# Kernel optimization log

Hardware: AMD Instinct MI355X
Metric: run time of the kernel (lower is better)

## Reference

```python
import jax, jax.numpy as jnp
import numpy as np

N, E, H, K, C, NMOD = 50000, 600000, 128, 5, 60, 12  # nodes, edges, hidden, hops, classes, 6 blocks * 2 modules


def setup_inputs() -> dict:
    key = jax.random.key(0)
    ks = iter(jax.random.split(key, 48))
    def rn(shape, scale=0.05):
        return jax.random.normal(next(ks), shape, jnp.float32) * scale
    return {
        "node_features": rn((N, 2), 1.0),
        "lap_pe": rn((N, K), 1.0),
        "edge_feat": rn((E, 4), 1.0),
        "src": jax.random.randint(next(ks), (E,), 0, N),
        "dst": jax.random.randint(next(ks), (E,), 0, N),
        "in_w": rn((2, H)), "in_b": jnp.zeros((H,), jnp.float32),
        "pos_w": rn((K, H)), "pos_b": jnp.zeros((H,), jnp.float32),
        "edge_w": rn((4, H)), "edge_b": jnp.zeros((H,), jnp.float32),
        "conv_w": rn((NMOD, 2, (K + 1) * H, H)), "conv_b": jnp.zeros((NMOD, 2, H), jnp.float32),
        "bn_g": jnp.ones((NMOD, 2, H), jnp.float32), "bn_b": jnp.zeros((NMOD, 2, H), jnp.float32),
        "ff_w": rn((NMOD, H, H)), "ff_b": jnp.zeros((NMOD, H), jnp.float32),
        "pose_w1": rn((H, H)), "pose_b1": jnp.zeros((H,), jnp.float32),
        "pose_w2": rn((H, 3)), "pose_b2": jnp.zeros((3,), jnp.float32),
        "lab_w1": rn((H, H)), "lab_b1": jnp.zeros((H,), jnp.float32),
        "lab_w2": rn((H, C)), "lab_b2": jnp.zeros((C,), jnp.float32),
    }


def _bn(x, g, b):
    # BatchNorm1d in training mode: stats over node axis
    m = x.mean(0)
    v = x.var(0)
    return (x - m) * jax.lax.rsqrt(v + 1e-5) * g + b


def reference(node_features, lap_pe, edge_feat, src, dst,
              in_w, in_b, pos_w, pos_b, edge_w, edge_b,
              conv_w, conv_b, bn_g, bn_b, ff_w, ff_b,
              pose_w1, pose_b1, pose_w2, pose_b2,
              lab_w1, lab_b1, lab_w2, lab_b2):
    seg = jax.ops.segment_sum
    # symmetric degree norm (in-degree, clamped to 1) as in DGL TAGConv
    deg = seg(jnp.ones((E,), node_features.dtype), dst, num_segments=N)
    norm = jnp.clip(deg, 1.0) ** -0.5  # [N]

    # edge feature aggregation: copy_e -> sum onto dst
    agg_e = seg(edge_feat @ edge_w + edge_b, dst, num_segments=N)  # [N,H]
    h = node_features @ in_w + in_b + lap_pe @ pos_w + pos_b + agg_e

    def tagconv(x, W, b):
        # fstack = [x, Ax, ..., A^K x] with A = D^-1/2 A D^-1/2, then single linear
        fs = [x]
        for _ in range(K):
            z = fs[-1] * norm[:, None]
            z = seg(z[src], dst, num_segments=N) * norm[:, None]
            fs.append(z)
        return jnp.concatenate(fs, axis=-1) @ W + b  # [N,H]

    for m in range(NMOD):  # 6 blocks x 2 TAGConvModules, sequential
        h_in = h
        h = jax.nn.relu(_bn(tagconv(h, conv_w[m, 0], conv_b[m, 0]), bn_g[m, 0], bn_b[m, 0]))
        h = jax.nn.relu(_bn(tagconv(h, conv_w[m, 1], conv_b[m, 1]), bn_g[m, 1], bn_b[m, 1]))
        h = h @ ff_w[m] + ff_b[m] + h_in  # dropout = identity (eval)

    pose = jax.nn.relu(h @ pose_w1 + pose_b1) @ pose_w2 + pose_b2  # [N,3]
    y = h.mean(0)  # dgl.mean_nodes (single batched graph)
    labels = jax.nn.relu(y @ lab_w1 + lab_b1) @ lab_w2 + lab_b2  # [C]
    return pose, labels
```

## Files before the change

### kernel.cpp

```cpp
#include <hip/hip_runtime.h>

#define NN 50000
#define EE 600000
#define HH 128
#define KK 5
#define CC 60
#define NMODS 12
#define MAXPE 750080
#define SC_NB 49

typedef _Float16 f16;
typedef __attribute__((ext_vector_type(8))) _Float16 f16x8;
typedef __attribute__((ext_vector_type(4))) _Float16 f16x4;
typedef __attribute__((ext_vector_type(16))) float f32x16;
typedef __attribute__((ext_vector_type(4))) int int4v;
typedef __attribute__((ext_vector_type(4))) float f32x4;

#define ZSL ((size_t)NN * 128)

#define GLOBAL_AS __attribute__((address_space(1)))
#define LDS_AS __attribute__((address_space(3)))


__global__ void k_deg(const int* __restrict__ dst, int* __restrict__ deg) {
    int i = blockIdx.x * 256 + threadIdx.x;
    if (i < EE) atomicAdd(&deg[dst[i]], 1);
}

__global__ __launch_bounds__(256) void k_scan1(const int* __restrict__ deg,
                                               int* __restrict__ rs, int* __restrict__ bsum) {
    __shared__ int sm[256];
    int t = threadIdx.x;
    int base = blockIdx.x * 1024 + t * 4;
    int d[4];
#pragma unroll
    for (int j = 0; j < 4; j++) {
        int i = base + j;
        d[j] = (i < NN) ? ((deg[i] + 3) & ~3) : 0;
    }
    int sum = d[0] + d[1] + d[2] + d[3];
    sm[t] = sum;
    __syncthreads();
    for (int off = 1; off < 256; off <<= 1) {
        int v = (t >= off) ? sm[t - off] : 0;
        __syncthreads();
        sm[t] += v;
        __syncthreads();
    }
    int excl = sm[t] - sum;
    int run = excl;
#pragma unroll
    for (int j = 0; j < 4; j++) {
        int i = base + j;
        if (i < NN) rs[i] = run;
        run += d[j];
    }
    if (t == 255) bsum[blockIdx.x] = sm[t];
}

__global__ __launch_bounds__(64) void k_scan2(const int* __restrict__ bsum, int* __restrict__ binc) {
    int l = threadIdx.x;
    int v = (l < SC_NB) ? bsum[l] : 0;
#pragma unroll
    for (int off = 1; off < 64; off <<= 1) {
        int tv = __shfl_up(v, off, 64);
        if (l >= off) v += tv;
    }
    binc[l] = v;
}

__global__ __launch_bounds__(256) void k_scan3(const int* __restrict__ binc, int* __restrict__ rs) {
    int i = blockIdx.x * 256 + threadIdx.x;
    if (i < NN) {
        int b = i >> 10;
        if (b > 0) rs[i] += binc[b - 1];
    } else if (i == NN) {
        rs[NN] = binc[SC_NB - 1];
    }
}

__global__ void k_norm(const int* __restrict__ deg, float* __restrict__ norm) {
    int i = blockIdx.x * 256 + threadIdx.x;
    if (i < NN) {
        int d = deg[i];
        float fd = (float)(d < 1 ? 1 : d);
        norm[i] = 1.0f / sqrtf(fd);
    }
}

__global__ void k_fill(const int* __restrict__ src, const int* __restrict__ dst,
                       const int* __restrict__ rs, const float* __restrict__ norm,
                       int* __restrict__ cursor,
                       int* __restrict__ csrc, float* __restrict__ ew, int* __restrict__ ceid) {
    int i = blockIdx.x * 256 + threadIdx.x;
    if (i >= EE) return;
    int d = dst[i];
    int slot = atomicAdd(&cursor[d], 1);
    int p = rs[d] + slot;
    int s = src[i];
    csrc[p] = s;
    ew[p] = norm[s];
    ceid[p] = i;
}


__global__ void k_cvtw(const float* __restrict__ conv_w, const float* __restrict__ ff_w,
                       const float* __restrict__ pose_w1,
                       f16* __restrict__ wc, f16* __restrict__ wf, f16* __restrict__ wp) {
    int i = blockIdx.x * 256 + threadIdx.x;
    const int NCW = 24 * 128 * 768;
    const int NFW = 12 * 128 * 128;
    const int NPW = 128 * 128;
    if (i < NCW) {
        int mat = i / (128 * 768); int rem = i - mat * (128 * 768);
        int col = rem / 768; int k = rem - col * 768;
        wc[i] = (f16)conv_w[(size_t)mat * 768 * 128 + (size_t)k * 128 + col];
    } else if (i < NCW + NFW) {
        int j = i - NCW;
        int mat = j / (128 * 128); int rem = j - mat * (128 * 128);
        int col = rem / 128; int k = rem - col * 128;
        wf[j] = (f16)ff_w[(size_t)mat * 128 * 128 + k * 128 + col];
    } else if (i < NCW + NFW + NPW) {
        int j = i - NCW - NFW;
        int col = j / 128; int k = j - col * 128;
        wp[j] = (f16)pose_w1[k * 128 + col];
    }
}


__global__ __launch_bounds__(128) void k_h0(
    const float* __restrict__ nf, const float* __restrict__ pe, const float* __restrict__ ef,
    const int* __restrict__ rs, const int* __restrict__ ceid, const float* __restrict__ ew,
    const int* __restrict__ deg,
    const float* __restrict__ in_w, const float* __restrict__ in_b,
    const float* __restrict__ pos_w, const float* __restrict__ pos_b,
    const float* __restrict__ edge_w, const float* __restrict__ edge_b,
    float* __restrict__ h, f16* __restrict__ zc) {
    int n = blockIdx.x;
    int f = threadIdx.x;
    float v = in_b[f] + pos_b[f];
    v += nf[n * 2 + 0] * in_w[f] + nf[n * 2 + 1] * in_w[HH + f];
#pragma unroll
    for (int k = 0; k < KK; k++) v += pe[n * KK + k] * pos_w[k * HH + f];
    float e0 = edge_w[f], e1 = edge_w[HH + f], e2 = edge_w[2 * HH + f], e3 = edge_w[3 * HH + f];
    int s = rs[n], e = rs[n + 1];
    v += (float)deg[n] * edge_b[f];
    for (int i = s; i < e; i++) {
        if (ew[i] == 0.f) continue;
        int eid = ceid[i];
        float4 x = ((const float4*)ef)[eid];
        v += x.x * e0 + x.y * e1 + x.z * e2 + x.w * e3;
    }
    h[(size_t)n * HH + f] = v;
    zc[(size_t)n * 128 + f] = (f16)v;
}


__global__ __launch_bounds__(256) void k_prop16(
    const f16* __restrict__ zin, f16* __restrict__ zout,
    const float* __restrict__ norm, const int* __restrict__ rs,
    const int* __restrict__ csrc, const float* __restrict__ ew) {
    int tid = threadIdx.x;
    int n = blockIdx.x * 16 + (tid >> 4);
    if (n >= NN) return;
    int c = (tid & 15) * 8;
    int s = rs[n], e = rs[n + 1];
    const f16* zp = zin + c;
    float acc[8] = {0.f, 0.f, 0.f, 0.f, 0.f, 0.f, 0.f, 0.f};
    for (int i = s; i < e; i += 4) {
        int4v id4 = __builtin_nontemporal_load((const int4v*)(csrc + i));
        f32x4 w4 = __builtin_nontemporal_load((const f32x4*)(ew + i));
        f16x8 v0 = *(const f16x8*)(zp + (size_t)id4.x * 128);
        f16x8 v1 = *(const f16x8*)(zp + (size_t)id4.y * 128);
        f16x8 v2 = *(const f16x8*)(zp + (size_t)id4.z * 128);
        f16x8 v3 = *(const f16x8*)(zp + (size_t)id4.w * 128);
#pragma unroll
        for (int j = 0; j < 8; j++)
            acc[j] += (float)v0[j] * w4.x + (float)v1[j] * w4.y +
                      (float)v2[j] * w4.z + (float)v3[j] * w4.w;
    }
    float nw = norm[n];
    f16x8 o;
#pragma unroll
    for (int j = 0; j < 8; j++) o[j] = (f16)(acc[j] * nw);
    *(f16x8*)(zout + (size_t)n * 128 + c) = o;
}


template <int KT, int BIAS, int RESID, int RELU, int WRZ>
__global__ __launch_bounds__(256) void k_mm(
    const f16* __restrict__ A, const f16* __restrict__ Wt,
    const float* __restrict__ bias, const float* __restrict__ Rsd,
    float* __restrict__ Y, f16* __restrict__ Zout) {
    __shared__ char smem[65536];
    char* As = smem;
    char* Bs = smem + 32768;
    int tid = threadIdx.x;
    int lane = tid & 63;
    int w = tid >> 6, wm = w >> 1, wn = w & 1;
    int n0 = blockIdx.x * 128;
    f32x16 acc[2][2] = {};
    for (int k0 = 0; k0 < KT; k0 += 128) {
        __syncthreads();
        const f16* Asl = A + (size_t)(k0 >> 7) * ZSL;
#pragma unroll
        for (int i = 0; i < 8; i++) {
            int p = (i * 256 + tid) * 16;
            int o = p ^ (((p >> 8) & 15) << 4);
            int r = o >> 8, ce = (o & 255) >> 1;
            int row = n0 + r; if (row >= NN) row = 0;
            const f16* ga = Asl + (size_t)row * 128 + ce;
            char* lba = As + i * 4096 + w * 1024;
            __builtin_amdgcn_global_load_lds((const GLOBAL_AS void*)ga, (LDS_AS void*)lba, 16, 0, 0);
            const f16* gb = Wt + (size_t)r * KT + k0 + ce;
            char* lbb = Bs + i * 4096 + w * 1024;
            __builtin_amdgcn_global_load_lds((const GLOBAL_AS void*)gb, (LDS_AS void*)lbb, 16, 0, 0);
        }
        asm volatile("s_waitcnt vmcnt(0)" ::: "memory");
        __syncthreads();
#pragma unroll
        for (int s = 0; s < 8; s++) {
            int koff = s * 32 + (lane >> 5) * 16;
            f16x8 a[2], b[2];
#pragma unroll
            for (int m = 0; m < 2; m++) {
                int rl = wm * 64 + m * 32 + (lane & 31);
                int oa = (rl * 256 + koff) ^ ((rl & 15) << 4);
                a[m] = *(const f16x8*)(As + oa);
                int cl = wn * 64 + m * 32 + (lane & 31);
                int ob = (cl * 256 + koff) ^ ((cl & 15) << 4);
                b[m] = *(const f16x8*)(Bs + ob);
            }
#pragma unroll
            for (int m = 0; m < 2; m++)
#pragma unroll
                for (int nb = 0; nb < 2; nb++)
                    acc[m][nb] = __builtin_amdgcn_mfma_f32_32x32x16_f16(a[m], b[nb], acc[m][nb], 0, 0, 0);
        }
    }
#pragma unroll
    for (int m = 0; m < 2; m++) {
        int rb = n0 + wm * 64 + m * 32 + 4 * (lane >> 5);
#pragma unroll
        for (int nb = 0; nb < 2; nb++) {
            int col = wn * 64 + nb * 32 + (lane & 31);
            float bv = 0.f;
            if (BIAS) bv = bias[col];
#pragma unroll
            for (int r = 0; r < 16; r++) {
                int row = rb + (r & 3) + 8 * (r >> 2);
                if (row >= NN) continue;
                float v = acc[m][nb][r] + bv;
                if (RESID) v += Rsd[(size_t)row * HH + col];
                if (RELU) v = fmaxf(v, 0.f);
                Y[(size_t)row * HH + col] = v;
                if (WRZ) Zout[(size_t)row * 128 + col] = (f16)v;
            }
        }
    }
}


__global__ __launch_bounds__(256) void k_bnstats(const float* __restrict__ Y, float* __restrict__ part) {
    int tid = threadIdx.x;
    float s = 0.f, q = 0.f;
    for (int n = blockIdx.x * 2 + (tid >> 7); n < NN; n += 512) {
        float v = Y[(size_t)n * HH + (tid & 127)];
        s += v; q += v * v;
    }
    __shared__ float sh[512];
    sh[tid] = s; sh[256 + tid] = q;
    __syncthreads();
    if (tid < 128) {
        part[blockIdx.x * 256 + tid] = sh[tid] + sh[tid + 128];
        part[blockIdx.x * 256 + 128 + tid] = sh[256 + tid] + sh[256 + tid + 128];
    }
}

__global__ __launch_bounds__(128) void k_bnfin(const float* __restrict__ part,
                                               const float* __restrict__ g, const float* __restrict__ b,
                                               float* __restrict__ sc, float* __restrict__ sh) {
    int f = threadIdx.x;
    float s = 0.f, q = 0.f;
    for (int bi = 0; bi < 256; bi++) {
        s += part[bi * 256 + f];
        q += part[bi * 256 + 128 + f];
    }
    float mean = s / (float)NN;
    float var = q / (float)NN - mean * mean;
    float scale = g[f] / sqrtf(var + 1e-5f);
    sc[f] = scale;
    sh[f] = b[f] - mean * scale;
}

__global__ __launch_bounds__(256) void k_bnapply(const float* __restrict__ Y,
                                                 const float* __restrict__ sc, const float* __restrict__ sh,
                                                 f16* __restrict__ zc) {
    int idx = blockIdx.x * 256 + threadIdx.x;
    if (idx >= NN * 32) return;
    float4 v = ((const float4*)Y)[idx];
    int c = idx & 31;
    float4 a = ((const float4*)sc)[c];
    float4 b = ((const float4*)sh)[c];
    int n = idx >> 5;
    f16x4 o;
    o[0] = (f16)fmaxf(v.x * a.x + b.x, 0.f);
    o[1] = (f16)fmaxf(v.y * a.y + b.y, 0.f);
    o[2] = (f16)fmaxf(v.z * a.z + b.z, 0.f);
    o[3] = (f16)fmaxf(v.w * a.w + b.w, 0.f);
    *(f16x4*)(zc + (size_t)n * 128 + c * 4) = o;
}


__global__ __launch_bounds__(128) void k_pose2(const float* __restrict__ T,
                                               const float* __restrict__ W2, const float* __restrict__ b2,
                                               float* __restrict__ out) {
    int tid = threadIdx.x;
    int n = blockIdx.x * 4 + (tid >> 5);
    int c = tid & 31;
    float4 tv = ((const float4*)T)[(size_t)n * 32 + c];
    float p0 = 0.f, p1 = 0.f, p2 = 0.f;
#pragma unroll
    for (int i = 0; i < 4; i++) {
        float t = (i == 0) ? tv.x : (i == 1) ? tv.y : (i == 2) ? tv.z : tv.w;
        int k = c * 4 + i;
        p0 += t * W2[k * 3 + 0];
        p1 += t * W2[k * 3 + 1];
        p2 += t * W2[k * 3 + 2];
    }
#pragma unroll
    for (int off = 16; off > 0; off >>= 1) {
        p0 += __shfl_down(p0, off, 32);
        p1 += __shfl_down(p1, off, 32);
        p2 += __shfl_down(p2, off, 32);
    }
    if (c == 0) {
        out[(size_t)n * 3 + 0] = p0 + b2[0];
        out[(size_t)n * 3 + 1] = p1 + b2[1];
        out[(size_t)n * 3 + 2] = p2 + b2[2];
    }
}

__global__ __launch_bounds__(256) void k_meanpart(const float* __restrict__ Y, float* __restrict__ part) {
    int tid = threadIdx.x;
    float s = 0.f;
    for (int n = blockIdx.x * 2 + (tid >> 7); n < NN; n += 512) {
        s += Y[(size_t)n * HH + (tid & 127)];
    }
    __shared__ float sh[256];
    sh[tid] = s;
    __syncthreads();
    if (tid < 128) part[blockIdx.x * 128 + tid] = sh[tid] + sh[tid + 128];
}

__global__ __launch_bounds__(128) void k_labels(const float* __restrict__ part,
                                                const float* __restrict__ w1, const float* __restrict__ b1,
                                                const float* __restrict__ w2, const float* __restrict__ b2,
                                                float* __restrict__ out) {
    __shared__ float ym[128];
    __shared__ float t2[128];
    int f = threadIdx.x;
    float s = 0.f;
    for (int bi = 0; bi < 256; bi++) s += part[bi * 128 + f];
    ym[f] = s / (float)NN;
    __syncthreads();
    float a = b1[f];
    for (int k = 0; k < 128; k++) a += ym[k] * w1[k * 128 + f];
    t2[f] = fmaxf(a, 0.f);
    __syncthreads();
    if (f < CC) {
        float a2 = b2[f];
        for (int k = 0; k < 128; k++) a2 += t2[k] * w2[k * CC + f];
        out[(size_t)NN * 3 + f] = a2;
    }
}


static inline size_t align256(size_t x) { return (x + 255) & ~(size_t)255; }

extern "C" void kernel_launch(void* const* d_in, const int* in_sizes, int n_in,
                              void* d_out, int out_size, void* d_ws, size_t ws_size,
                              hipStream_t stream) {
    const float* nf = (const float*)d_in[0];
    const float* pe = (const float*)d_in[1];
    const float* ef = (const float*)d_in[2];
    const int* src = (const int*)d_in[3];
    const int* dst = (const int*)d_in[4];
    const float* in_w = (const float*)d_in[5];
    const float* in_b = (const float*)d_in[6];
    const float* pos_w = (const float*)d_in[7];
    const float* pos_b = (const float*)d_in[8];
    const float* edge_w = (const float*)d_in[9];
    const float* edge_b = (const float*)d_in[10];
    const float* conv_w = (const float*)d_in[11];
    const float* bn_g = (const float*)d_in[13];
    const float* bn_b = (const float*)d_in[14];
    const float* ff_w = (const float*)d_in[15];
    const float* ff_b = (const float*)d_in[16];
    const float* pose_w1 = (const float*)d_in[17];
    const float* pose_b1 = (const float*)d_in[18];
    const float* pose_w2 = (const float*)d_in[19];
    const float* pose_b2 = (const float*)d_in[20];
    const float* lab_w1 = (const float*)d_in[21];
    const float* lab_b1 = (const float*)d_in[22];
    const float* lab_w2 = (const float*)d_in[23];
    const float* lab_b2 = (const float*)d_in[24];
    float* out = (float*)d_out;

    char* wsp = (char*)d_ws;
    size_t off = 0;
    auto alloc = [&](size_t bytes) -> void* {
        void* p = wsp + off;
        off += align256(bytes);
        return p;
    };
    float* norm = (float*)alloc((size_t)NN * 4);
    int* deg = (int*)alloc((size_t)NN * 4);
    int* rs = (int*)alloc((size_t)(NN + 1) * 4);
    int* cursor = (int*)alloc((size_t)NN * 4);
    int* csrc = (int*)alloc((size_t)MAXPE * 4);
    float* ew = (float*)alloc((size_t)MAXPE * 4);
    int* ceid = (int*)alloc((size_t)MAXPE * 4);
    int* bsum = (int*)alloc(64 * 4);
    int* binc = (int*)alloc(64 * 4);
    float* hin = (float*)alloc((size_t)NN * HH * 4);
    float* ybuf = (float*)alloc((size_t)NN * HH * 4);
    f16* zcat = (f16*)alloc((size_t)6 * ZSL * 2);
    f16* wc = (f16*)alloc((size_t)24 * 128 * 768 * 2);
    f16* wf = (f16*)alloc((size_t)12 * 128 * 128 * 2);
    f16* wp = (f16*)alloc((size_t)128 * 128 * 2);
    float* part = (float*)alloc(256 * 256 * 4);
    float* mpart = (float*)alloc(256 * 128 * 4);
    float* bnsc = (float*)alloc(128 * 4);
    float* bnsh = (float*)alloc(128 * 4);
    (void)ws_size; (void)in_sizes; (void)n_in; (void)out_size;

    hipMemsetAsync(deg, 0, (size_t)NN * 4, stream);
    hipMemsetAsync(cursor, 0, (size_t)NN * 4, stream);
    hipMemsetAsync(csrc, 0, (size_t)MAXPE * 4, stream);
    hipMemsetAsync(ew, 0, (size_t)MAXPE * 4, stream);
    int egrid = (EE + 255) / 256;
    k_deg<<<egrid, 256, 0, stream>>>(dst, deg);
    k_scan1<<<SC_NB, 256, 0, stream>>>(deg, rs, bsum);
    k_scan2<<<1, 64, 0, stream>>>(bsum, binc);
    k_scan3<<<(NN + 256) / 256, 256, 0, stream>>>(binc, rs);
    k_norm<<<(NN + 255) / 256, 256, 0, stream>>>(deg, norm);
    k_fill<<<egrid, 256, 0, stream>>>(src, dst, rs, norm, cursor, csrc, ew, ceid);

    const int NCVT = 24 * 128 * 768 + 12 * 128 * 128 + 128 * 128;
    k_cvtw<<<(NCVT + 255) / 256, 256, 0, stream>>>(conv_w, ff_w, pose_w1, wc, wf, wp);

    k_h0<<<NN, 128, 0, stream>>>(nf, pe, ef, rs, ceid, ew, deg, in_w, in_b, pos_w, pos_b,
                                 edge_w, edge_b, hin, zcat);

    const int mmgrid = (NN + 127) / 128;
    const int pgrid = (NN + 15) / 16;
    const int agrid = (NN * 32) / 256;

    for (int m = 0; m < NMODS; m++) {
        for (int s = 0; s < 2; s++) {
            const f16* Wb = wc + (size_t)(m * 2 + s) * 128 * 768;
            for (int k = 1; k <= KK; k++) {
                k_prop16<<<pgrid, 256, 0, stream>>>(zcat + (size_t)(k - 1) * ZSL,
                                                    zcat + (size_t)k * ZSL,
                                                    norm, rs, csrc, ew);
            }
            k_mm<768, 0, 0, 0, 0><<<mmgrid, 256, 0, stream>>>(zcat, Wb, nullptr, nullptr,
                                                              ybuf, nullptr);
            k_bnstats<<<256, 256, 0, stream>>>(ybuf, part);
            k_bnfin<<<1, 128, 0, stream>>>(part, bn_g + (size_t)(m * 2 + s) * HH,
                                           bn_b + (size_t)(m * 2 + s) * HH, bnsc, bnsh);
            k_bnapply<<<agrid, 256, 0, stream>>>(ybuf, bnsc, bnsh, zcat);
        }
        k_mm<128, 1, 1, 0, 1><<<mmgrid, 256, 0, stream>>>(zcat, wf + (size_t)m * 128 * 128,
                                                          ff_b + (size_t)m * HH, hin, hin, zcat);
    }

    k_mm<128, 1, 0, 1, 0><<<mmgrid, 256, 0, stream>>>(zcat, wp, pose_b1, nullptr, ybuf, nullptr);
    k_pose2<<<NN / 4, 128, 0, stream>>>(ybuf, pose_w2, pose_b2, out);

    k_meanpart<<<256, 256, 0, stream>>>(hin, mpart);
    k_labels<<<1, 128, 0, stream>>>(mpart, lab_w1, lab_b1, lab_w2, lab_b2, out);
}
```

Baseline: 5.194 ms.

## Fuse BatchNorm statistics into GEMM epilogue and split propagation over column slices

The conv GEMM epilogue now accumulates per-column sums and sums of squares, reduces them through shared memory and writes per-block partials. This removes the separate stats kernel that re-read the full output. The propagation kernel now maps 64 nodes by a 32-column slice per block across a 2D grid, which changes the gather access pattern and cache behaviour. The extra shared-memory reduction adds a little work to the GEMM, and the slice split may reduce coalescing of neighbour-row reads.

```diff
diff --git a/kernel.cpp b/kernel.cpp
--- a/kernel.cpp
+++ b/kernel.cpp
@@ -8,6 +8,7 @@
 #define NMODS 12
 #define MAXPE 750080
 #define SC_NB 49
+#define MMGRID 391
 
 typedef _Float16 f16;
 typedef __attribute__((ext_vector_type(8))) _Float16 f16x8;
@@ -161,9 +162,9 @@
     const float* __restrict__ norm, const int* __restrict__ rs,
     const int* __restrict__ csrc, const float* __restrict__ ew) {
     int tid = threadIdx.x;
-    int n = blockIdx.x * 16 + (tid >> 4);
+    int n = blockIdx.x * 64 + (tid >> 2);
     if (n >= NN) return;
-    int c = (tid & 15) * 8;
+    int c = blockIdx.y * 32 + (tid & 3) * 8;
     int s = rs[n], e = rs[n + 1];
     const f16* zp = zin + c;
     float acc[8] = {0.f, 0.f, 0.f, 0.f, 0.f, 0.f, 0.f, 0.f};
@@ -187,11 +188,11 @@
 }
 
 
-template <int KT, int BIAS, int RESID, int RELU, int WRZ>
+template <int KT, int BIAS, int RESID, int RELU, int WRZ, int STATS>
 __global__ __launch_bounds__(256) void k_mm(
     const f16* __restrict__ A, const f16* __restrict__ Wt,
     const float* __restrict__ bias, const float* __restrict__ Rsd,
-    float* __restrict__ Y, f16* __restrict__ Zout) {
+    float* __restrict__ Y, f16* __restrict__ Zout, float* __restrict__ part) {
     __shared__ char smem[65536];
     char* As = smem;
     char* Bs = smem + 32768;
@@ -238,6 +239,7 @@
                     acc[m][nb] = __builtin_amdgcn_mfma_f32_32x32x16_f16(a[m], b[nb], acc[m][nb], 0, 0, 0);
         }
     }
+    float ssum[2] = {0.f, 0.f}, sqq[2] = {0.f, 0.f};
 #pragma unroll
     for (int m = 0; m < 2; m++) {
         int rb = n0 + wm * 64 + m * 32 + 4 * (lane >> 5);
@@ -253,36 +255,34 @@
                 float v = acc[m][nb][r] + bv;
                 if (RESID) v += Rsd[(size_t)row * HH + col];
                 if (RELU) v = fmaxf(v, 0.f);
+                if (STATS) { ssum[nb] += v; sqq[nb] += v * v; }
                 Y[(size_t)row * HH + col] = v;
                 if (WRZ) Zout[(size_t)row * 128 + col] = (f16)v;
             }
         }
     }
-}
-
-
-__global__ __launch_bounds__(256) void k_bnstats(const float* __restrict__ Y, float* __restrict__ part) {
-    int tid = threadIdx.x;
-    float s = 0.f, q = 0.f;
-    for (int n = blockIdx.x * 2 + (tid >> 7); n < NN; n += 512) {
-        float v = Y[(size_t)n * HH + (tid & 127)];
-        s += v; q += v * v;
-    }
-    __shared__ float sh[512];
-    sh[tid] = s; sh[256 + tid] = q;
-    __syncthreads();
-    if (tid < 128) {
-        part[blockIdx.x * 256 + tid] = sh[tid] + sh[tid + 128];
-        part[blockIdx.x * 256 + 128 + tid] = sh[256 + tid] + sh[256 + tid + 128];
-    }
-}
+    if (STATS) {
+        __syncthreads();
+        float* red = (float*)smem;
+        int slot = wm * 2 + (lane >> 5);
+        int colb = wn * 64 + (lane & 31);
+        red[slot * 256 + colb] = ssum[0];
+        red[slot * 256 + colb + 32] = ssum[1];
+        red[slot * 256 + 128 + colb] = sqq[0];
+        red[slot * 256 + 128 + colb + 32] = sqq[1];
+        __syncthreads();
+        float t = red[tid] + red[256 + tid] + red[512 + tid] + red[768 + tid];
+        part[blockIdx.x * 256 + tid] = t;
+    }
+}
+
 
 __global__ __launch_bounds__(128) void k_bnfin(const float* __restrict__ part,
                                                const float* __restrict__ g, const float* __restrict__ b,
                                                float* __restrict__ sc, float* __restrict__ sh) {
     int f = threadIdx.x;
     float s = 0.f, q = 0.f;
-    for (int bi = 0; bi < 256; bi++) {
+    for (int bi = 0; bi < MMGRID; bi++) {
         s += part[bi * 256 + f];
         q += part[bi * 256 + 128 + f];
     }
@@ -429,7 +429,7 @@
     f16* wc = (f16*)alloc((size_t)24 * 128 * 768 * 2);
     f16* wf = (f16*)alloc((size_t)12 * 128 * 128 * 2);
     f16* wp = (f16*)alloc((size_t)128 * 128 * 2);
-    float* part = (float*)alloc(256 * 256 * 4);
+    float* part = (float*)alloc((size_t)MMGRID * 256 * 4);
     float* mpart = (float*)alloc(256 * 128 * 4);
     float* bnsc = (float*)alloc(128 * 4);
     float* bnsh = (float*)alloc(128 * 4);
@@ -453,8 +453,7 @@
     k_h0<<<NN, 128, 0, stream>>>(nf, pe, ef, rs, ceid, ew, deg, in_w, in_b, pos_w, pos_b,
                                  edge_w, edge_b, hin, zcat);
 
-    const int mmgrid = (NN + 127) / 128;
-    const int pgrid = (NN + 15) / 16;
+    const dim3 pgrid((NN + 63) / 64, 4);
     const int agrid = (NN * 32) / 256;
 
     for (int m = 0; m < NMODS; m++) {
@@ -465,18 +464,19 @@
                                                     zcat + (size_t)k * ZSL,
                                                     norm, rs, csrc, ew);
             }
-            k_mm<768, 0, 0, 0, 0><<<mmgrid, 256, 0, stream>>>(zcat, Wb, nullptr, nullptr,
-                                                              ybuf, nullptr);
-            k_bnstats<<<256, 256, 0, stream>>>(ybuf, part);
+            k_mm<768, 0, 0, 0, 0, 1><<<MMGRID, 256, 0, stream>>>(zcat, Wb, nullptr, nullptr,
+                                                                 ybuf, nullptr, part);
             k_bnfin<<<1, 128, 0, stream>>>(part, bn_g + (size_t)(m * 2 + s) * HH,
                                            bn_b + (size_t)(m * 2 + s) * HH, bnsc, bnsh);
             k_bnapply<<<agrid, 256, 0, stream>>>(ybuf, bnsc, bnsh, zcat);
         }
-        k_mm<128, 1, 1, 0, 1><<<mmgrid, 256, 0, stream>>>(zcat, wf + (size_t)m * 128 * 128,
-                                                          ff_b + (size_t)m * HH, hin, hin, zcat);
-    }
-
-    k_mm<128, 1, 0, 1, 0><<<mmgrid, 256, 0, stream>>>(zcat, wp, pose_b1, nullptr, ybuf, nullptr);
+        k_mm<128, 1, 1, 0, 1, 0><<<MMGRID, 256, 0, stream>>>(zcat, wf + (size_t)m * 128 * 128,
+                                                             ff_b + (size_t)m * HH, hin, hin,
+                                                             zcat, nullptr);
+    }
+
+    k_mm<128, 1, 0, 1, 0, 0><<<MMGRID, 256, 0, stream>>>(zcat, wp, pose_b1, nullptr, ybuf,
+                                                         nullptr, nullptr);
     k_pose2<<<NN / 4, 128, 0, stream>>>(ybuf, pose_w2, pose_b2, out);
 
     k_meanpart<<<256, 256, 0, stream>>>(hin, mpart);
```

Result: slower. 7.109 ms (+36.9%).
